# Performance work log

Measured on AMD Instinct MI355X. Metric: run time of the kernel, lower is better.

The kernel has to match this reference:

```python
import jax, jax.numpy as jnp
import numpy as np

FILTER_LEN = 1024
HOP_LEN = 256


def _forward_basis(filter_len):
    half = filter_len // 2 + 1
    basis = np.fft.fft(np.eye(filter_len))
    basis = np.vstack([np.real(basis[:half, :]), np.imag(basis[:half, :])])
    # hann window, fftbins=True (periodic)
    n = np.arange(filter_len)
    win = 0.5 - 0.5 * np.cos(2.0 * np.pi * n / filter_len)
    return (basis * win).astype(np.float32)  # [2*half, filter_len]


def setup_inputs() -> dict:
    key = jax.random.key(0)
    x = jax.random.normal(key, (8, 1048576), dtype=jnp.float32)
    basis = jnp.asarray(_forward_basis(FILTER_LEN))[:, None, :]  # [O=1026, I=1, K=1024]
    return {"x": x, "basis": basis}


def reference(x, basis):
    pad = FILTER_LEN // 2
    # [B, 1, T + filter_len] with reflect padding on the time axis
    xp = jnp.pad(x[:, None, :], ((0, 0), (0, 0), (pad, pad)), mode="reflect")
    # strided conv1d against the fixed DFT basis -> [B, 1026, n_frames]
    out = jax.lax.conv_general_dilated(
        xp, basis,
        window_strides=(HOP_LEN,),
        padding="VALID",
        dimension_numbers=("NCH", "OIH", "NCH"),
    )
    return out
```

## Files before the change

kernel.cpp:

```cpp
#include <hip/hip_runtime.h>
#include <hip/hip_bf16.h>

#define T_LEN 1048576
#define FL    1024
#define PADL  512
#define HOP   256
#define NFR   4097
#define NB    8
#define XP2   1049600
#define NSEG  4100
#define MROWS 1028
#define MPAD  1152
#define MTL   9
#define FTL   34
#define NTL   272
#define NWG2  2448

typedef __bf16 bf16x8 __attribute__((ext_vector_type(8)));
typedef float  f32x4  __attribute__((ext_vector_type(4)));

__device__ __forceinline__ void gload16(const __hip_bfloat16* g, void* l) {
  __builtin_amdgcn_global_load_lds(
      (const __attribute__((address_space(1))) unsigned int*)g,
      (__attribute__((address_space(3))) unsigned int*)l, 16, 0, 0);
}

__global__ __launch_bounds__(256) void pad_convert_x8(
    const float* __restrict__ x, __hip_bfloat16* __restrict__ xp) {
  const int base = (blockIdx.x * 256 + threadIdx.x) * 8;
  const int b = blockIdx.y;
  if (base >= XP2) return;
  const float* __restrict__ xb = x + (size_t)b * T_LEN;
  union { bf16x8 v; __hip_bfloat16 h[8]; } o;
  if (base >= PADL && base + 8 <= PADL + T_LEN) {
    const float4 v0 = *(const float4*)&xb[base - PADL];
    const float4 v1 = *(const float4*)&xb[base - PADL + 4];
    o.h[0] = __float2bfloat16(v0.x); o.h[1] = __float2bfloat16(v0.y);
    o.h[2] = __float2bfloat16(v0.z); o.h[3] = __float2bfloat16(v0.w);
    o.h[4] = __float2bfloat16(v1.x); o.h[5] = __float2bfloat16(v1.y);
    o.h[6] = __float2bfloat16(v1.z); o.h[7] = __float2bfloat16(v1.w);
    *(bf16x8*)&xp[(size_t)b * XP2 + base] = o.v;
  } else {
    for (int e = 0; e < 8; ++e) {
      const int i = base + e;
      if (i < XP2) {
        const int t = i - PADL;
        const int idx = (t < 0) ? -t : ((t >= T_LEN) ? (2 * T_LEN - 2 - t) : t);
        xp[(size_t)b * XP2 + i] = __float2bfloat16(xb[idx]);
      }
    }
  }
}

__global__ __launch_bounds__(256) void build_cmat(__hip_bfloat16* __restrict__ cm) {
  const int idx = blockIdx.x * 256 + threadIdx.x;
  if (idx >= MPAD * 256) return;
  const int row = idx >> 8, r = idx & 255;
  float v = 0.f;
  if (row < MROWS) {
    const int k = row >> 1;
    const int ph = (k * r) & 1023;
    const float ang = (float)ph * 6.2831853071795864769f / 1024.f;
    v = (row & 1) ? -sinf(ang) : cosf(ang);
  }
  cm[idx] = __float2bfloat16(v);
}

__global__ __launch_bounds__(512, 2) void stft_fgemm(
    const __hip_bfloat16* __restrict__ Cm,
    const __hip_bfloat16* __restrict__ X,
    float* __restrict__ out) {
  __shared__ char ldsraw[128 * 132 * 4];
  __hip_bfloat16* stg = (__hip_bfloat16*)ldsraw;
  float* Ub = (float*)ldsraw;

  const int orig = blockIdx.x;
  const int wg = (orig & 7) * (NWG2 / 8) + (orig >> 3);
  const int mt = wg % MTL;
  const int nt = wg / MTL;
  const int b = nt / FTL, ft = nt % FTL;
  const int gb = ft * 124;
  const int RB = mt * 124;
  const int kbase = 62 * mt;

  const int tid = threadIdx.x;
  const int w = tid >> 6, l = tid & 63;
  const bool isProd = w >= 4;
  const int cw = w & 3;
  const int wm = cw >> 1, wn = cw & 1;

  const int g_log = (l & 3) ^ ((l >> 3) & 3);
  const int srow = l >> 2;
  const __hip_bfloat16* aB_[2];
  const __hip_bfloat16* bB_[2];
#pragma unroll
  for (int j = 0; j < 2; ++j) {
    const int c = cw * 2 + j;
    aB_[j] = Cm + (size_t)(RB + c * 16 + srow) * 256 + g_log * 8;
    int g = gb + c * 16 + srow;
    if (g > NSEG - 1) g = NSEG - 1;
    bB_[j] = X + (size_t)b * XP2 + (size_t)g * 256 + g_log * 8;
  }

  const int swz = ((l >> 4) ^ ((l >> 1) & 3)) * 8;
  const int aIdx = (wm * 64 + (l & 15)) * 32 + swz;
  const int bIdx = 4096 + (wn * 64 + (l & 15)) * 32 + swz;

  f32x4 acc[4][4] = {};

#define STAGE(K0_, S_) do {                                                  \
    _Pragma("unroll") for (int j = 0; j < 2; ++j) {                          \
      const int c_ = cw * 2 + j;                                             \
      gload16(aB_[j] + (K0_), (void*)(stg + (S_) * 8192 + c_ * 512));        \
      gload16(bB_[j] + (K0_), (void*)(stg + (S_) * 8192 + 4096 + c_ * 512)); \
    }                                                                        \
  } while (0)

#define RDMM(S_) do {                                                        \
    bf16x8 af_[4], bf_[4];                                                   \
    _Pragma("unroll") for (int m = 0; m < 4; ++m)                            \
      af_[m] = *(const bf16x8*)(stg + (S_) * 8192 + aIdx + m * 512);         \
    _Pragma("unroll") for (int n = 0; n < 4; ++n)                            \
      bf_[n] = *(const bf16x8*)(stg + (S_) * 8192 + bIdx + n * 512);         \
    __builtin_amdgcn_s_setprio(1);                                           \
    _Pragma("unroll") for (int m = 0; m < 4; ++m)                            \
      _Pragma("unroll") for (int n = 0; n < 4; ++n)                          \
        acc[m][n] = __builtin_amdgcn_mfma_f32_16x16x32_bf16(                 \
            af_[m], bf_[n], acc[m][n], 0, 0, 0);                             \
    __builtin_amdgcn_s_setprio(0);                                           \
  } while (0)

#define BAR __builtin_amdgcn_s_barrier()
#define SB  __builtin_amdgcn_sched_barrier(0)
#define VMC(N_) asm volatile("s_waitcnt vmcnt(" #N_ ")" ::: "memory")

  if (isProd) {
    STAGE(0, 0); STAGE(32, 1); STAGE(64, 2); STAGE(96, 3);
    VMC(8);  BAR;
    VMC(0);  BAR;
    SB; STAGE(128, 0); STAGE(160, 1);
    VMC(0);  BAR;
    SB; STAGE(192, 2); STAGE(224, 3);
    VMC(0);  BAR;
  } else {
    BAR;
    SB; RDMM(0); RDMM(1); BAR;
    SB; RDMM(2); RDMM(3); BAR;
    SB; RDMM(0); RDMM(1); BAR;
    SB; RDMM(2); RDMM(3);
  }
  __syncthreads();

#undef VMC
#undef SB
#undef RDMM
#undef STAGE

  if (!isProd) {
    const int cb = l & 15, rb2 = (l >> 4) * 4;
#pragma unroll
    for (int m = 0; m < 4; ++m)
#pragma unroll
      for (int n = 0; n < 4; ++n) {
        const int row = wm * 64 + m * 16 + rb2;
        const int col = wn * 64 + n * 16 + cb;
#pragma unroll
        for (int jj = 0; jj < 4; ++jj)
          Ub[(row + jj) * 132 + col] = acc[m][n][jj];
      }
  }
  __syncthreads();

  f32x4 zre[4], zim[4];
#pragma unroll
  for (int it = 0; it < 4; ++it) {
    const int cell = it * 512 + tid;
    const int rp = cell >> 5;
    const int g4 = (cell & 31) * 4;
    const float* rr = Ub + (rp * 2) * 132 + g4;
    const f32x4 r0 = *(const f32x4*)rr;
    const f32x4 r1 = *(const f32x4*)(rr + 4);
    const f32x4 i0 = *(const f32x4*)(rr + 132);
    const f32x4 i1 = *(const f32x4*)(rr + 136);
    const float ur[8] = {r0[0], r0[1], r0[2], r0[3], r1[0], r1[1], r1[2], r1[3]};
    const float ui[8] = {i0[0], i0[1], i0[2], i0[3], i1[0], i1[1], i1[2], i1[3]};
    const int cls = (kbase + rp) & 3;
    const float s = (cls & 2) ? -1.f : 1.f;
    const bool odd = cls & 1;
    f32x4 zr, zi;
#pragma unroll
    for (int j = 0; j < 4; ++j) {
      const float p  = ur[j] - ur[j + 2], q  = ur[j] + ur[j + 2];
      const float pi = ui[j] - ui[j + 2], qi = ui[j] + ui[j + 2];
      const float rm = ur[j + 1] - ur[j + 3], rp_ = ur[j + 1] + ur[j + 3];
      const float sm = ui[j + 1] - ui[j + 3], sp = ui[j + 1] + ui[j + 3];
      zr[j] = odd ? (p + s * sm) : (q + s * rp_);
      zi[j] = odd ? (pi - s * rm) : (qi + s * sp);
    }
    zre[it] = zr; zim[it] = zi;
  }
  __syncthreads();
#pragma unroll
  for (int it = 0; it < 4; ++it) {
    const int cell = it * 512 + tid;
    const int rp = cell >> 5;
    const int g4 = (cell & 31) * 4;
    *(f32x4*)(Ub + (rp * 2) * 132 + g4) = zre[it];
    *(f32x4*)(Ub + (rp * 2 + 1) * 132 + g4) = zim[it];
  }
  __syncthreads();

  const size_t ob = (size_t)b * 1026 * 4097;
#pragma unroll
  for (int it = 0; it < 4; ++it) {
    const int cell = it * 512 + tid;
    const int rp = cell >> 5;
    const int g4 = (cell & 31) * 4;
    const int k = kbase + rp;
    const int f0 = gb + g4;
    if (g4 <= 120) {
      if (rp >= 1 && rp <= 62 && k <= 512) {
        const float* zp = Ub + rp * 264 + g4;
        const f32x4 zmr = *(const f32x4*)(zp - 264);
        const f32x4 zmi = *(const f32x4*)(zp - 132);
        const f32x4 zpr = *(const f32x4*)(zp + 264);
        const f32x4 zpi = *(const f32x4*)(zp + 396);
        const f32x4 Yr = 0.5f * zre[it] - 0.25f * (zmr + zpr);
        const f32x4 Yi = 0.5f * zim[it] - 0.25f * (zmi + zpi);
        float* orow = out + ob + (size_t)k * NFR;
        float* irow = out + ob + (size_t)(513 + k) * NFR;
        if (f0 + 3 <= NFR - 1) {
          *(f32x4*)&orow[f0] = Yr;
          *(f32x4*)&irow[f0] = Yi;
        } else {
#pragma unroll
          for (int j = 0; j < 4; ++j)
            if (f0 + j <= NFR - 1) { orow[f0 + j] = Yr[j]; irow[f0 + j] = Yi[j]; }
        }
      } else if (mt == 0 && rp == 0) {
        const f32x4 z1r = *(const f32x4*)(Ub + 264 + g4);
        const f32x4 Yr = 0.5f * zre[it] - 0.5f * z1r;
        const f32x4 Yi = 0.5f * zim[it];
        if (f0 + 3 <= NFR - 1) {
          *(f32x4*)&out[ob + f0] = Yr;
          *(f32x4*)&out[ob + (size_t)513 * NFR + f0] = Yi;
        } else {
#pragma unroll
          for (int j = 0; j < 4; ++j)
            if (f0 + j <= NFR - 1) {
              out[ob + f0 + j] = Yr[j];
              out[ob + (size_t)513 * NFR + f0 + j] = Yi[j];
            }
        }
      }
    }
  }
#undef BAR
}

extern "C" void kernel_launch(void* const* d_in, const int* in_sizes, int n_in,
                              void* d_out, int out_size, void* d_ws, size_t ws_size,
                              hipStream_t stream) {
  const float* x = (const float*)d_in[0];
  float* out = (float*)d_out;

  __hip_bfloat16* xpBf = (__hip_bfloat16*)d_ws;
  __hip_bfloat16* cmat = xpBf + (size_t)NB * XP2;

  dim3 gPad((XP2 / 8 + 255) / 256, NB);
  pad_convert_x8<<<gPad, 256, 0, stream>>>(x, xpBf);

  build_cmat<<<(MPAD * 256) / 256, 256, 0, stream>>>(cmat);

  stft_fgemm<<<NWG2, 512, 0, stream>>>(cmat, xpBf, out);
}
```

Measured before the change: 59.29 us.

## Fuse reflect-pad and bf16 conversion into GEMM producer loads

Removes the separate pad/convert kernel and its bf16 workspace round-trip. Producer waves now read fp32 input directly, handle the reflect edges with per-element indexing, convert to bf16 in registers and write to LDS. This saves a kernel launch and roughly 16MB of write plus read traffic. In exchange, the producer loads now go through registers instead of direct-to-LDS, and each fp32 sample is read by several overlapping frames.

```diff
diff --git a/kernel.cpp b/kernel.cpp
--- a/kernel.cpp
+++ b/kernel.cpp
@@ -7,7 +7,6 @@
 #define HOP   256
 #define NFR   4097
 #define NB    8
-#define XP2   1049600
 #define NSEG  4100
 #define MROWS 1028
 #define MPAD  1152
@@ -23,33 +22,6 @@
   __builtin_amdgcn_global_load_lds(
       (const __attribute__((address_space(1))) unsigned int*)g,
       (__attribute__((address_space(3))) unsigned int*)l, 16, 0, 0);
-}
-
-__global__ __launch_bounds__(256) void pad_convert_x8(
-    const float* __restrict__ x, __hip_bfloat16* __restrict__ xp) {
-  const int base = (blockIdx.x * 256 + threadIdx.x) * 8;
-  const int b = blockIdx.y;
-  if (base >= XP2) return;
-  const float* __restrict__ xb = x + (size_t)b * T_LEN;
-  union { bf16x8 v; __hip_bfloat16 h[8]; } o;
-  if (base >= PADL && base + 8 <= PADL + T_LEN) {
-    const float4 v0 = *(const float4*)&xb[base - PADL];
-    const float4 v1 = *(const float4*)&xb[base - PADL + 4];
-    o.h[0] = __float2bfloat16(v0.x); o.h[1] = __float2bfloat16(v0.y);
-    o.h[2] = __float2bfloat16(v0.z); o.h[3] = __float2bfloat16(v0.w);
-    o.h[4] = __float2bfloat16(v1.x); o.h[5] = __float2bfloat16(v1.y);
-    o.h[6] = __float2bfloat16(v1.z); o.h[7] = __float2bfloat16(v1.w);
-    *(bf16x8*)&xp[(size_t)b * XP2 + base] = o.v;
-  } else {
-    for (int e = 0; e < 8; ++e) {
-      const int i = base + e;
-      if (i < XP2) {
-        const int t = i - PADL;
-        const int idx = (t < 0) ? -t : ((t >= T_LEN) ? (2 * T_LEN - 2 - t) : t);
-        xp[(size_t)b * XP2 + i] = __float2bfloat16(xb[idx]);
-      }
-    }
-  }
 }
 
 __global__ __launch_bounds__(256) void build_cmat(__hip_bfloat16* __restrict__ cm) {
@@ -68,7 +40,7 @@
 
 __global__ __launch_bounds__(512, 2) void stft_fgemm(
     const __hip_bfloat16* __restrict__ Cm,
-    const __hip_bfloat16* __restrict__ X,
+    const float* __restrict__ x,
     float* __restrict__ out) {
   __shared__ char ldsraw[128 * 132 * 4];
   __hip_bfloat16* stg = (__hip_bfloat16*)ldsraw;
@@ -91,15 +63,20 @@
 
   const int g_log = (l & 3) ^ ((l >> 3) & 3);
   const int srow = l >> 2;
+  const float* __restrict__ xb = x + (size_t)b * T_LEN;
   const __hip_bfloat16* aB_[2];
-  const __hip_bfloat16* bB_[2];
+  long boff[2];
+  int edgeC[2];
+  bool intr[2];
 #pragma unroll
   for (int j = 0; j < 2; ++j) {
     const int c = cw * 2 + j;
     aB_[j] = Cm + (size_t)(RB + c * 16 + srow) * 256 + g_log * 8;
     int g = gb + c * 16 + srow;
     if (g > NSEG - 1) g = NSEG - 1;
-    bB_[j] = X + (size_t)b * XP2 + (size_t)g * 256 + g_log * 8;
+    intr[j] = (g >= 2 && g <= 4097);
+    boff[j] = (long)g * 256 - 512 + g_log * 8;
+    edgeC[j] = (g <= 1 ? 512 - g * 256 : 2097662 - g * 256) - g_log * 8;
   }
 
   const int swz = ((l >> 4) ^ ((l >> 1) & 3)) * 8;
@@ -108,11 +85,38 @@
 
   f32x4 acc[4][4] = {};
 
-#define STAGE(K0_, S_) do {                                                  \
+#define STAGE_A(K0_, S_) do {                                                \
+    _Pragma("unroll") for (int j = 0; j < 2; ++j)                            \
+      gload16(aB_[j] + (K0_), (void*)(stg + (S_) * 8192 + (cw*2 + j)*512));  \
+  } while (0)
+
+#define LDB(K0_, F_) do {                                                    \
     _Pragma("unroll") for (int j = 0; j < 2; ++j) {                          \
-      const int c_ = cw * 2 + j;                                             \
-      gload16(aB_[j] + (K0_), (void*)(stg + (S_) * 8192 + c_ * 512));        \
-      gload16(bB_[j] + (K0_), (void*)(stg + (S_) * 8192 + 4096 + c_ * 512)); \
+      if (intr[j]) {                                                         \
+        F_[j*2]   = *(const float4*)&xb[boff[j] + (K0_)];                    \
+        F_[j*2+1] = *(const float4*)&xb[boff[j] + (K0_) + 4];                \
+      } else {                                                               \
+        const int c0_ = edgeC[j] - (K0_);                                    \
+        F_[j*2].x   = xb[c0_];     F_[j*2].y   = xb[c0_ - 1];                \
+        F_[j*2].z   = xb[c0_ - 2]; F_[j*2].w   = xb[c0_ - 3];                \
+        F_[j*2+1].x = xb[c0_ - 4]; F_[j*2+1].y = xb[c0_ - 5];                \
+        F_[j*2+1].z = xb[c0_ - 6]; F_[j*2+1].w = xb[c0_ - 7];                \
+      }                                                                      \
+    }                                                                        \
+  } while (0)
+
+#define WRB(S_, F_) do {                                                     \
+    _Pragma("unroll") for (int j = 0; j < 2; ++j) {                          \
+      union { bf16x8 v; __hip_bfloat16 h[8]; } u_;                           \
+      u_.h[0] = __float2bfloat16(F_[j*2].x);                                 \
+      u_.h[1] = __float2bfloat16(F_[j*2].y);                                 \
+      u_.h[2] = __float2bfloat16(F_[j*2].z);                                 \
+      u_.h[3] = __float2bfloat16(F_[j*2].w);                                 \
+      u_.h[4] = __float2bfloat16(F_[j*2+1].x);                               \
+      u_.h[5] = __float2bfloat16(F_[j*2+1].y);                               \
+      u_.h[6] = __float2bfloat16(F_[j*2+1].z);                               \
+      u_.h[7] = __float2bfloat16(F_[j*2+1].w);                               \
+      *(bf16x8*)(stg + (S_)*8192 + 4096 + (cw*2 + j)*512 + l*8) = u_.v;      \
     }                                                                        \
   } while (0)
 
@@ -132,16 +136,21 @@
 
 #define BAR __builtin_amdgcn_s_barrier()
 #define SB  __builtin_amdgcn_sched_barrier(0)
-#define VMC(N_) asm volatile("s_waitcnt vmcnt(" #N_ ")" ::: "memory")
+#define VMC0 asm volatile("s_waitcnt vmcnt(0)" ::: "memory")
+#define LGKM0 asm volatile("s_waitcnt lgkmcnt(0)" ::: "memory")
 
   if (isProd) {
-    STAGE(0, 0); STAGE(32, 1); STAGE(64, 2); STAGE(96, 3);
-    VMC(8);  BAR;
-    VMC(0);  BAR;
-    SB; STAGE(128, 0); STAGE(160, 1);
-    VMC(0);  BAR;
-    SB; STAGE(192, 2); STAGE(224, 3);
-    VMC(0);  BAR;
+    float4 B0[4], B1[4], B2[4], B3[4];
+    STAGE_A(0, 0); STAGE_A(32, 1); STAGE_A(64, 2); STAGE_A(96, 3);
+    LDB(0, B0); LDB(32, B1); LDB(64, B2); LDB(96, B3);
+    VMC0;
+    WRB(0, B0); WRB(1, B1); WRB(2, B2); WRB(3, B3);
+    LGKM0; BAR;
+    BAR;
+    SB; STAGE_A(128, 0); STAGE_A(160, 1); LDB(128, B0); LDB(160, B1);
+    VMC0; WRB(0, B0); WRB(1, B1); LGKM0; BAR;
+    SB; STAGE_A(192, 2); STAGE_A(224, 3); LDB(192, B2); LDB(224, B3);
+    VMC0; WRB(2, B2); WRB(3, B3); LGKM0; BAR;
   } else {
     BAR;
     SB; RDMM(0); RDMM(1); BAR;
@@ -151,10 +160,13 @@
   }
   __syncthreads();
 
-#undef VMC
+#undef VMC0
+#undef LGKM0
 #undef SB
 #undef RDMM
-#undef STAGE
+#undef WRB
+#undef LDB
+#undef STAGE_A
 
   if (!isProd) {
     const int cb = l & 15, rb2 = (l >> 4) * 4;
@@ -264,13 +276,9 @@
   const float* x = (const float*)d_in[0];
   float* out = (float*)d_out;
 
-  __hip_bfloat16* xpBf = (__hip_bfloat16*)d_ws;
-  __hip_bfloat16* cmat = xpBf + (size_t)NB * XP2;
-
-  dim3 gPad((XP2 / 8 + 255) / 256, NB);
-  pad_convert_x8<<<gPad, 256, 0, stream>>>(x, xpBf);
+  __hip_bfloat16* cmat = (__hip_bfloat16*)d_ws;
 
   build_cmat<<<(MPAD * 256) / 256, 256, 0, stream>>>(cmat);
 
-  stft_fgemm<<<NWG2, 512, 0, stream>>>(cmat, xpBf, out);
-}
+  stft_fgemm<<<NWG2, 512, 0, stream>>>(cmat, x, out);
+}
```

Measured after the change: 101.5 us. 1.71x slower.
